# Optimization experiments

Hardware: AMD Instinct MI355X
Metric: run time of the kernel (lower is better)

The kernel has to match this reference:

```python
import jax, jax.numpy as jnp
import numpy as np

B, N, DIM = 4, 2048, 128
K = 32            # num_nearest_neighbors
FF = 4            # fourier_features
M_DIM = 16
EDGE_IN = FF * 2 + DIM * 2 + 1  # 265


def setup_inputs() -> dict:
    key = jax.random.key(0)
    ks = jax.random.split(key, 16)
    std = 0.001  # init_eps normal init for Linear weights
    p = {
        "feats": jax.random.normal(ks[0], (B, N, DIM), jnp.float32),
        "coors": jax.random.normal(ks[1], (B, N, 3), jnp.float32),
        # edge_mlp: Linear(265, 530) -> SiLU -> Linear(530, 16) -> SiLU
        "eW1": jax.random.normal(ks[2], (EDGE_IN, EDGE_IN * 2), jnp.float32) * std,
        "eb1": jax.random.normal(ks[3], (EDGE_IN * 2,), jnp.float32) * std,
        "eW2": jax.random.normal(ks[4], (EDGE_IN * 2, M_DIM), jnp.float32) * std,
        "eb2": jax.random.normal(ks[5], (M_DIM,), jnp.float32) * std,
        # coors_mlp: Linear(16, 64) -> SiLU -> Linear(64, 1)
        "cW1": jax.random.normal(ks[6], (M_DIM, M_DIM * 4), jnp.float32) * std,
        "cb1": jax.random.normal(ks[7], (M_DIM * 4,), jnp.float32) * std,
        "cW2": jax.random.normal(ks[8], (M_DIM * 4, 1), jnp.float32) * std,
        "cb2": jax.random.normal(ks[9], (1,), jnp.float32) * std,
        # node_mlp: Linear(144, 256) -> SiLU -> Linear(256, 128)
        "nW1": jax.random.normal(ks[10], (DIM + M_DIM, DIM * 2), jnp.float32) * std,
        "nb1": jax.random.normal(ks[11], (DIM * 2,), jnp.float32) * std,
        "nW2": jax.random.normal(ks[12], (DIM * 2, DIM), jnp.float32) * std,
        "nb2": jax.random.normal(ks[13], (DIM,), jnp.float32) * std,
    }
    return p


def _egnn_fwd(feats, coors, eW1, eb1, eW2, eb2, cW1, cb1, cW2, cb2, nW1, nb1, nW2, nb2):
    # all-pairs squared distances: [b, n, n]
    rel_coors_full = coors[:, :, None, :] - coors[:, None, :, :]
    rel_dist = jnp.sum(rel_coors_full * rel_coors_full, axis=-1)

    # top-k nearest (smallest distance) -> indices [b, n, k]
    _, idx = jax.lax.top_k(-rel_dist, K)

    # gather neighbor coords / feats per batch: [b, n, k, *]
    coors_j = jax.vmap(lambda x, i: x[i])(coors, idx)
    feats_j = jax.vmap(lambda x, i: x[i])(feats, idx)
    rel_coors = coors[:, :, None, :] - coors_j                     # b n k 3
    d = jnp.take_along_axis(rel_dist, idx, axis=2)[..., None]       # b n k 1

    # fourier encode distances: [b, n, k, 2*FF + 1]
    scales = 2.0 ** jnp.arange(FF, dtype=feats.dtype)               # [FF]
    xs = d[..., None] / scales                                      # b n k 1 FF
    enc = jnp.concatenate([jnp.sin(xs), jnp.cos(xs), d[..., None]], axis=-1)
    enc = enc[..., 0, :]                                            # b n k (2FF+1)

    feats_i = jnp.broadcast_to(feats[:, :, None, :], feats_j.shape)
    edge_input = jnp.concatenate([feats_i, feats_j, enc], axis=-1)  # b n k 265

    # edge MLP -> messages m_ij [b, n, k, m_dim]
    h = jax.nn.silu(edge_input @ eW1 + eb1)
    m_ij = jax.nn.silu(h @ eW2 + eb2)

    # coors MLP -> per-edge coordinate weights [b, n, k]
    cw = (jax.nn.silu(m_ij @ cW1 + cb1) @ cW2 + cb2)[..., 0]
    coors_out = jnp.einsum('bij,bijc->bic', cw, rel_coors) + coors

    # node update: sum-pool messages, concat with feats, MLP + residual
    m_i = jnp.sum(m_ij, axis=-2)                                    # b n m_dim
    node_in = jnp.concatenate([feats, m_i], axis=-1)
    node_out = jax.nn.silu(node_in @ nW1 + nb1) @ nW2 + nb2 + feats
    return node_out, coors_out


def reference(feats, coors, eW1, eb1, eW2, eb2, cW1, cb1, cW2, cb2, nW1, nb1, nW2, nb2):
    return _egnn_fwd(feats, coors, eW1, eb1, eW2, eb2, cW1, cb1, cW2, cb2, nW1, nb1, nW2, nb2)
```

## Files before the change

### kernel.cpp

```cpp
#include <hip/hip_runtime.h>
#include <hip/hip_bf16.h>
#include <math.h>

#define Bb 4
#define Nn 2048
#define DIMd 128
#define Kk 32
#define H1 530
#define PW2 530
#define MD 16
#define NDH 256
#define NDI 144
#define HSP 552

typedef float f32x2 __attribute__((ext_vector_type(2)));
typedef float f32x4 __attribute__((ext_vector_type(4)));
typedef short s16x8 __attribute__((ext_vector_type(8)));

__device__ __forceinline__ unsigned short f2bf(float f){
    union { float f; unsigned u; } v; v.f = f;
    unsigned r = v.u + 0x7FFFu + ((v.u >> 16) & 1u);
    return (unsigned short)(r >> 16);
}
__device__ __forceinline__ float silu_f(float x){
    float e = __builtin_amdgcn_exp2f(x * -1.442695041f);
    return x * __builtin_amdgcn_rcpf(1.0f + e);
}
__device__ __forceinline__ f32x2 silu2(f32x2 x){
    float e0 = __builtin_amdgcn_exp2f(x[0] * -1.442695041f);
    float e1 = __builtin_amdgcn_exp2f(x[1] * -1.442695041f);
    f32x2 r;
    r[0] = x[0] * __builtin_amdgcn_rcpf(1.0f + e0);
    r[1] = x[1] * __builtin_amdgcn_rcpf(1.0f + e1);
    return r;
}
__device__ __forceinline__ unsigned cvt_pk_bf16(float a, float b){
    unsigned r;
    asm("v_cvt_pk_bf16_f32 %0, %1, %2" : "=v"(r) : "v"(a), "v"(b));
    return r;
}

__global__ __launch_bounds__(256) void topk_kernel(const float* __restrict__ coors,
        int* __restrict__ idx_ws, float* __restrict__ dv_ws){
    int tid = threadIdx.x;
    int w = tid >> 6, lane = tid & 63;
    int node = blockIdx.x * 4 + w;
    int b = node >> 11;
    const float* cbp = coors + (size_t)b * Nn * 3;
    float cx = coors[node*3+0], cy = coors[node*3+1], cz = coors[node*3+2];
    float d[32];
    #pragma unroll
    for (int t = 0; t < 32; t++){
        int j = t*64 + lane;
        float dx = cx - cbp[j*3+0], dy = cy - cbp[j*3+1], dz = cz - cbp[j*3+2];
        d[t] = dx*dx + dy*dy + dz*dz;
    }
    float md = d[0]; int mj = lane;
    #pragma unroll
    for (int t = 1; t < 32; t++){
        int jt = t*64 + lane;
        if (d[t] < md){ md = d[t]; mj = jt; }
    }
    for (int r = 0; r < Kk; r++){
        float bd = md; int bj = mj;
        #pragma unroll
        for (int off = 32; off; off >>= 1){
            float d2 = __shfl_xor(bd, off); int j2 = __shfl_xor(bj, off);
            if (d2 < bd || (d2 == bd && j2 < bj)){ bd = d2; bj = j2; }
        }
        if (lane == 0){
            idx_ws[node*Kk + r] = bj;
            dv_ws[node*Kk + r] = bd;
        }
        if (mj == bj){
            md = 3.4e38f; mj = 0x7fffffff;
            #pragma unroll
            for (int t = 0; t < 32; t++){
                int jt = t*64 + lane;
                if (jt == bj) d[t] = 3.4e38f;
                if (d[t] < md){ md = d[t]; mj = jt; }
            }
        }
    }
}

__global__ __launch_bounds__(256) void fragw_kernel(const float* __restrict__ eW1,
        const float* __restrict__ eW2,
        unsigned short* __restrict__ W1F, unsigned short* __restrict__ WPF,
        unsigned short* __restrict__ W2F){
    int i0 = blockIdx.x * 256 + threadIdx.x;
    int stride = gridDim.x * 256;
    for (int i = i0; i < 34*5*512; i += stride){
        int j = i & 7, lane = (i >> 3) & 63, t = i >> 9;
        int ks = t % 5, nt = t / 5;
        int cg = nt*16 + (lane & 15);
        int k = ks*32 + ((lane >> 4) << 3) + j;
        float v = 0.f;
        if (cg < H1){
            if (k < 128) v = eW1[(size_t)(128+k)*H1 + cg];
            else if (k < 137) v = eW1[(size_t)(256+(k-128))*H1 + cg];
        }
        W1F[i] = f2bf(v);
    }
    for (int i = i0; i < 34*4*512; i += stride){
        int j = i & 7, lane = (i >> 3) & 63, t = i >> 9;
        int ks = t & 3, nt = t >> 2;
        int cg = nt*16 + (lane & 15);
        int k = ks*32 + ((lane >> 4) << 3) + j;
        float v = (cg < H1) ? eW1[(size_t)k*H1 + cg] : 0.f;
        WPF[i] = f2bf(v);
    }
    for (int i = i0; i < 17*512; i += stride){
        int j = i & 7, lane = (i >> 3) & 63, s = i >> 9;
        int k = s*32 + ((lane >> 4) << 3) + j;
        int col = lane & 15;
        W2F[i] = (k < H1) ? f2bf(eW2[(size_t)k*MD + col]) : (unsigned short)0;
    }
}

__global__ __launch_bounds__(256) void pmat_kernel(const float* __restrict__ feats,
        const unsigned short* __restrict__ WPF, const float* __restrict__ eb1,
        float* __restrict__ P){
    int tid = threadIdx.x;
    int wid = tid >> 6, lane = tid & 63;
    int node0 = blockIdx.x * 32;
    int kg = (lane >> 4) * 8;
    s16x8 af[2][4];
    #pragma unroll
    for (int m = 0; m < 2; m++){
        const float* fr = feats + (size_t)(node0 + m*16 + (lane & 15)) * DIMd;
        #pragma unroll
        for (int ks = 0; ks < 4; ks++){
            f32x4 lo = *(const f32x4*)(fr + ks*32 + kg);
            f32x4 hi = *(const f32x4*)(fr + ks*32 + kg + 4);
            union { s16x8 v; unsigned u[4]; } pk;
            pk.u[0] = cvt_pk_bf16(lo[0], lo[1]); pk.u[1] = cvt_pk_bf16(lo[2], lo[3]);
            pk.u[2] = cvt_pk_bf16(hi[0], hi[1]); pk.u[3] = cvt_pk_bf16(hi[2], hi[3]);
            af[m][ks] = pk.v;
        }
    }
    const s16x8* WPFv = (const s16x8*)WPF;
    for (int nt = wid; nt < 34; nt += 4){
        f32x4 acc0 = {0,0,0,0}, acc1 = {0,0,0,0};
        #pragma unroll
        for (int ks = 0; ks < 4; ks++){
            s16x8 bb = WPFv[(nt*4 + ks)*64 + lane];
            acc0 = __builtin_amdgcn_mfma_f32_16x16x32_bf16(af[0][ks], bb, acc0, 0, 0, 0);
            acc1 = __builtin_amdgcn_mfma_f32_16x16x32_bf16(af[1][ks], bb, acc1, 0, 0, 0);
        }
        int cg = nt*16 + (lane & 15);
        if (cg < H1){
            float b = eb1[cg];
            int r0 = (lane >> 4) * 4;
            #pragma unroll
            for (int r = 0; r < 4; r++){
                P[(size_t)(node0 + r0 + r)*PW2 + cg]      = acc0[r] + b;
                P[(size_t)(node0 + 16 + r0 + r)*PW2 + cg] = acc1[r] + b;
            }
        }
    }
}

__global__ __launch_bounds__(256, 4) void edge_kernel(const float* __restrict__ coors,
        const float* __restrict__ feats, const float* __restrict__ eb2,
        const float* __restrict__ cW1, const float* __restrict__ cb1,
        const float* __restrict__ cW2, const float* __restrict__ cb2,
        const float* __restrict__ P, const unsigned short* __restrict__ W1F,
        const unsigned short* __restrict__ W2F,
        const int* __restrict__ idx_ws, const float* __restrict__ dv_ws,
        float* __restrict__ mi_ws, float* __restrict__ coors_out){
    __shared__ unsigned short Hs[Kk][HSP];
    __shared__ float Pi_lds[544];
    __shared__ __align__(16) unsigned short aenc[Kk][32];
    __shared__ int js[Kk];
    __shared__ float rels[Kk][3];
    __shared__ float cacc[4][3];
    float (*m_s)[MD] = (float (*)[MD])aenc;

    int node = blockIdx.x; int tid = threadIdx.x;
    int b = node >> 11;
    int wid = tid >> 6, lane = tid & 63;

    const float* Pn = P + (size_t)node*PW2;
    Pi_lds[tid]       = Pn[tid];
    Pi_lds[tid + 256] = (tid + 256 < PW2) ? Pn[tid + 256] : 0.f;
    if (tid < 32) Pi_lds[512 + tid] = (512 + tid < PW2) ? Pn[512 + tid] : 0.f;
    if (tid < Kk){
        int j = idx_ws[node*Kk + tid];
        float dv = dv_ws[node*Kk + tid];
        js[tid] = j;
        unsigned short e[9];
        e[0] = f2bf(sinf(dv));        e[1] = f2bf(sinf(dv*0.5f));
        e[2] = f2bf(sinf(dv*0.25f));  e[3] = f2bf(sinf(dv*0.125f));
        e[4] = f2bf(cosf(dv));        e[5] = f2bf(cosf(dv*0.5f));
        e[6] = f2bf(cosf(dv*0.25f));  e[7] = f2bf(cosf(dv*0.125f));
        e[8] = f2bf(dv);
        #pragma unroll
        for (int q = 0; q < 9; q++) aenc[tid][q] = e[q];
        #pragma unroll
        for (int q = 9; q < 32; q++) aenc[tid][q] = 0;
        int jg = (b << 11) + j;
        rels[tid][0] = coors[node*3+0] - coors[jg*3+0];
        rels[tid][1] = coors[node*3+1] - coors[jg*3+1];
        rels[tid][2] = coors[node*3+2] - coors[jg*3+2];
    }
    __syncthreads();

    int kg = (lane >> 4) * 8;
    s16x8 af[2][5];
    #pragma unroll
    for (int m = 0; m < 2; m++){
        int row = m*16 + (lane & 15);
        int jgl = (b << 11) + js[row];
        const float* fr = feats + (size_t)jgl * DIMd;
        #pragma unroll
        for (int ks = 0; ks < 4; ks++){
            f32x4 lo = *(const f32x4*)(fr + ks*32 + kg);
            f32x4 hi = *(const f32x4*)(fr + ks*32 + kg + 4);
            union { s16x8 v; unsigned u[4]; } pk;
            pk.u[0] = cvt_pk_bf16(lo[0], lo[1]); pk.u[1] = cvt_pk_bf16(lo[2], lo[3]);
            pk.u[2] = cvt_pk_bf16(hi[0], hi[1]); pk.u[3] = cvt_pk_bf16(hi[2], hi[3]);
            af[m][ks] = pk.v;
        }
        af[m][4] = *(const s16x8*)(&aenc[row][kg]);
    }

    const s16x8* W1Fv = (const s16x8*)W1F;
    for (int nt = wid; nt < 34; nt += 4){
        f32x4 acc0 = {0,0,0,0}, acc1 = {0,0,0,0};
        #pragma unroll
        for (int ks = 0; ks < 5; ks++){
            s16x8 bb = W1Fv[(nt*5 + ks)*64 + lane];
            acc0 = __builtin_amdgcn_mfma_f32_16x16x32_bf16(af[0][ks], bb, acc0, 0, 0, 0);
            acc1 = __builtin_amdgcn_mfma_f32_16x16x32_bf16(af[1][ks], bb, acc1, 0, 0, 0);
        }
        int cg = nt*16 + (lane & 15);
        bool valid = cg < H1;
        float pic = Pi_lds[cg];
        int r0 = (lane >> 4) * 4;
        #pragma unroll
        for (int r = 0; r < 4; r++){
            float x0 = acc0[r] + pic, x1 = acc1[r] + pic;
            Hs[r0 + r][cg]      = valid ? f2bf(silu_f(x0)) : (unsigned short)0;
            Hs[16 + r0 + r][cg] = valid ? f2bf(silu_f(x1)) : (unsigned short)0;
        }
    }
    __syncthreads();

    if (wid < 2){
        f32x4 acc = {0.f,0.f,0.f,0.f};
        int ar = wid*16 + (lane & 15);
        const s16x8* W2Fv = (const s16x8*)W2F;
        for (int s = 0; s < 17; s++){
            s16x8 a  = *(const s16x8*)(&Hs[ar][s*32 + kg]);
            s16x8 bb = W2Fv[s*64 + lane];
            acc = __builtin_amdgcn_mfma_f32_16x16x32_bf16(a, bb, acc, 0, 0, 0);
        }
        int col = lane & 15, r0 = (lane >> 4) * 4;
        #pragma unroll
        for (int r = 0; r < 4; r++) m_s[wid*16 + r0 + r][col] = acc[r];
    }
    __syncthreads();
    for (int t = tid; t < Kk*MD; t += 256){
        int n = t >> 4, f = t & 15;
        m_s[n][f] = silu_f(m_s[n][f] + eb2[f]);
    }
    __syncthreads();
    if (tid < MD){
        float s = 0.f;
        for (int n = 0; n < Kk; n++) s += m_s[n][tid];
        mi_ws[node*MD + tid] = s;
    }
    float ax = 0.f, ay = 0.f, az = 0.f;
    for (int q = 0; q < 8; q++){
        int n = wid*8 + q;
        float acc = cb1[lane];
        #pragma unroll
        for (int f = 0; f < MD; f++) acc += m_s[n][f] * cW1[f*64 + lane];
        float p = silu_f(acc) * cW2[lane];
        #pragma unroll
        for (int off = 32; off; off >>= 1) p += __shfl_xor(p, off);
        float cw = p + cb2[0];
        ax += cw * rels[n][0];
        ay += cw * rels[n][1];
        az += cw * rels[n][2];
    }
    if (lane == 0){ cacc[wid][0] = ax; cacc[wid][1] = ay; cacc[wid][2] = az; }
    __syncthreads();
    if (tid == 0){
        coors_out[node*3+0] = cacc[0][0]+cacc[1][0]+cacc[2][0]+cacc[3][0] + coors[node*3+0];
        coors_out[node*3+1] = cacc[0][1]+cacc[1][1]+cacc[2][1]+cacc[3][1] + coors[node*3+1];
        coors_out[node*3+2] = cacc[0][2]+cacc[1][2]+cacc[2][2]+cacc[3][2] + coors[node*3+2];
    }
}

__global__ __launch_bounds__(256) void node_kernel(const float* __restrict__ feats,
        const float* __restrict__ mi_ws,
        const float* __restrict__ nW1, const float* __restrict__ nb1,
        const float* __restrict__ nW2, const float* __restrict__ nb2,
        float* __restrict__ out){
    __shared__ float insT[NDI][12];
    __shared__ float hsdT[NDH][12];
    int tid = threadIdx.x;
    int node0 = blockIdx.x * 8;
    for (int t = tid; t < 8*DIMd; t += 256){
        int m = t >> 7, k = t & 127;
        insT[k][m] = feats[(size_t)node0*DIMd + t];
    }
    if (tid < 8*MD) insT[DIMd + (tid & 15)][tid >> 4] = mi_ws[node0*MD + tid];
    __syncthreads();
    float bias = nb1[tid];
    f32x2 acc[4];
    #pragma unroll
    for (int p = 0; p < 4; p++) acc[p] = (f32x2){bias, bias};
    for (int k = 0; k < NDI; k++){
        float wv = nW1[(size_t)k*NDH + tid];
        f32x2 w2 = {wv, wv};
        acc[0] += *(const f32x2*)&insT[k][0] * w2;
        acc[1] += *(const f32x2*)&insT[k][2] * w2;
        acc[2] += *(const f32x2*)&insT[k][4] * w2;
        acc[3] += *(const f32x2*)&insT[k][6] * w2;
    }
    #pragma unroll
    for (int p = 0; p < 4; p++) *(f32x2*)&hsdT[tid][2*p] = silu2(acc[p]);
    __syncthreads();
    int c = tid & 127, half = tid >> 7;
    float b2 = nb2[c];
    f32x2 a0 = {b2, b2}, a1 = {b2, b2};
    for (int k = 0; k < NDH; k++){
        float wv = nW2[(size_t)k*DIMd + c];
        f32x2 w2 = {wv, wv};
        a0 += *(const f32x2*)&hsdT[k][half*4]     * w2;
        a1 += *(const f32x2*)&hsdT[k][half*4 + 2] * w2;
    }
    #pragma unroll
    for (int q = 0; q < 4; q++){
        int m = half*4 + q;
        float v = (q < 2) ? a0[q & 1] : a1[q & 1];
        out[(size_t)(node0+m)*DIMd + c] = v + feats[(size_t)(node0+m)*DIMd + c];
    }
}

extern "C" void kernel_launch(void* const* d_in, const int* in_sizes, int n_in,
                              void* d_out, int out_size, void* d_ws, size_t ws_size,
                              hipStream_t stream){
    const float* feats = (const float*)d_in[0];
    const float* coors = (const float*)d_in[1];
    const float* eW1 = (const float*)d_in[2];
    const float* eb1 = (const float*)d_in[3];
    const float* eW2 = (const float*)d_in[4];
    const float* eb2 = (const float*)d_in[5];
    const float* cW1 = (const float*)d_in[6];
    const float* cb1 = (const float*)d_in[7];
    const float* cW2 = (const float*)d_in[8];
    const float* cb2 = (const float*)d_in[9];
    const float* nW1 = (const float*)d_in[10];
    const float* nb1 = (const float*)d_in[11];
    const float* nW2 = (const float*)d_in[12];
    const float* nb2 = (const float*)d_in[13];
    float* out = (float*)d_out;
    float* coors_out = out + (size_t)Bb*Nn*DIMd;

    char* ws = (char*)d_ws;
    int*   idx_ws = (int*)ws;
    float* dv_ws  = (float*)(ws + (1u<<20));
    float* Pd     = (float*)(ws + (2u<<20));
    float* mi_ws  = (float*)(ws + (2u<<20) + 17367040u);
    unsigned short* W1F = (unsigned short*)(ws + (2u<<20) + 17367040u + 524288u);
    unsigned short* WPF = (unsigned short*)(ws + (2u<<20) + 17367040u + 524288u + 174080u);
    unsigned short* W2F = (unsigned short*)(ws + (2u<<20) + 17367040u + 524288u + 174080u + 139264u);

    fragw_kernel<<<256, 256, 0, stream>>>(eW1, eW2, W1F, WPF, W2F);
    pmat_kernel<<<Bb*Nn/32, 256, 0, stream>>>(feats, WPF, eb1, Pd);
    topk_kernel<<<Bb*Nn/4, 256, 0, stream>>>(coors, idx_ws, dv_ws);
    edge_kernel<<<Bb*Nn, 256, 0, stream>>>(coors, feats, eb2, cW1, cb1, cW2, cb2,
                                           Pd, W1F, W2F, idx_ws, dv_ws, mi_ws, coors_out);
    node_kernel<<<Bb*Nn/8, 256, 0, stream>>>(feats, mi_ws, nW1, nb1, nW2, nb2, out);
}
```

Baseline: 305.0 us.

## Split edge kernel into two half-neighbor blocks per node with partial-sum combine

Each node's 32 neighbors are now handled by two blocks of 16 edges. Each block writes partial message sums and partial coordinate updates, and a new combine kernel plus the node kernel add the two halves together. The change halves per-block LDS and registers, raises the occupancy hint to 8, stores the P bias row as bf16, and vectorises the coors-MLP across 16-lane groups. The cost is that every W1 fragment load now feeds only one MFMA instead of two, which doubles W1 global traffic, and an extra kernel launch is added. Rounding the bias to bf16 also adds precision loss.

```diff
diff --git a/kernel.cpp b/kernel.cpp
--- a/kernel.cpp
+++ b/kernel.cpp
@@ -21,6 +21,10 @@
     union { float f; unsigned u; } v; v.f = f;
     unsigned r = v.u + 0x7FFFu + ((v.u >> 16) & 1u);
     return (unsigned short)(r >> 16);
+}
+__device__ __forceinline__ float bf2f(unsigned short u){
+    union { unsigned u; float f; } v; v.u = ((unsigned)u) << 16;
+    return v.f;
 }
 __device__ __forceinline__ float silu_f(float x){
     float e = __builtin_amdgcn_exp2f(x * -1.442695041f);
@@ -161,33 +165,35 @@
     }
 }
 
-__global__ __launch_bounds__(256, 4) void edge_kernel(const float* __restrict__ coors,
+__global__ __launch_bounds__(256, 8) void edge_kernel(const float* __restrict__ coors,
         const float* __restrict__ feats, const float* __restrict__ eb2,
         const float* __restrict__ cW1, const float* __restrict__ cb1,
         const float* __restrict__ cW2, const float* __restrict__ cb2,
         const float* __restrict__ P, const unsigned short* __restrict__ W1F,
         const unsigned short* __restrict__ W2F,
         const int* __restrict__ idx_ws, const float* __restrict__ dv_ws,
-        float* __restrict__ mi_ws, float* __restrict__ coors_out){
-    __shared__ unsigned short Hs[Kk][HSP];
-    __shared__ float Pi_lds[544];
-    __shared__ __align__(16) unsigned short aenc[Kk][32];
-    __shared__ int js[Kk];
-    __shared__ float rels[Kk][3];
+        float* __restrict__ mi_part, float* __restrict__ co_part){
+    __shared__ unsigned short Hs[16][HSP];
+    __shared__ unsigned short Pi_bf[544];
+    __shared__ __align__(16) unsigned short aenc[16][32];
+    __shared__ int js[16];
+    __shared__ float rels[16][3];
     __shared__ float cacc[4][3];
     float (*m_s)[MD] = (float (*)[MD])aenc;
 
-    int node = blockIdx.x; int tid = threadIdx.x;
+    int bid = blockIdx.x;
+    int node = bid >> 1, h = bid & 1;
     int b = node >> 11;
+    int tid = threadIdx.x;
     int wid = tid >> 6, lane = tid & 63;
 
     const float* Pn = P + (size_t)node*PW2;
-    Pi_lds[tid]       = Pn[tid];
-    Pi_lds[tid + 256] = (tid + 256 < PW2) ? Pn[tid + 256] : 0.f;
-    if (tid < 32) Pi_lds[512 + tid] = (512 + tid < PW2) ? Pn[512 + tid] : 0.f;
-    if (tid < Kk){
-        int j = idx_ws[node*Kk + tid];
-        float dv = dv_ws[node*Kk + tid];
+    Pi_bf[tid] = f2bf(Pn[tid]);
+    { int c = tid + 256; Pi_bf[c] = (c < PW2) ? f2bf(Pn[c]) : (unsigned short)0; }
+    if (tid < 32){ int c = 512 + tid; Pi_bf[c] = (c < PW2) ? f2bf(Pn[c]) : (unsigned short)0; }
+    if (tid < 16){
+        int j = idx_ws[node*Kk + h*16 + tid];
+        float dv = dv_ws[node*Kk + h*16 + tid];
         js[tid] = j;
         unsigned short e[9];
         e[0] = f2bf(sinf(dv));        e[1] = f2bf(sinf(dv*0.5f));
@@ -207,10 +213,9 @@
     __syncthreads();
 
     int kg = (lane >> 4) * 8;
-    s16x8 af[2][5];
-    #pragma unroll
-    for (int m = 0; m < 2; m++){
-        int row = m*16 + (lane & 15);
+    int row = lane & 15;
+    s16x8 af[5];
+    {
         int jgl = (b << 11) + js[row];
         const float* fr = feats + (size_t)jgl * DIMd;
         #pragma unroll
@@ -220,36 +225,32 @@
             union { s16x8 v; unsigned u[4]; } pk;
             pk.u[0] = cvt_pk_bf16(lo[0], lo[1]); pk.u[1] = cvt_pk_bf16(lo[2], lo[3]);
             pk.u[2] = cvt_pk_bf16(hi[0], hi[1]); pk.u[3] = cvt_pk_bf16(hi[2], hi[3]);
-            af[m][ks] = pk.v;
-        }
-        af[m][4] = *(const s16x8*)(&aenc[row][kg]);
+            af[ks] = pk.v;
+        }
+        af[4] = *(const s16x8*)(&aenc[row][kg]);
     }
 
     const s16x8* W1Fv = (const s16x8*)W1F;
     for (int nt = wid; nt < 34; nt += 4){
-        f32x4 acc0 = {0,0,0,0}, acc1 = {0,0,0,0};
+        f32x4 acc = {0,0,0,0};
         #pragma unroll
         for (int ks = 0; ks < 5; ks++){
             s16x8 bb = W1Fv[(nt*5 + ks)*64 + lane];
-            acc0 = __builtin_amdgcn_mfma_f32_16x16x32_bf16(af[0][ks], bb, acc0, 0, 0, 0);
-            acc1 = __builtin_amdgcn_mfma_f32_16x16x32_bf16(af[1][ks], bb, acc1, 0, 0, 0);
+            acc = __builtin_amdgcn_mfma_f32_16x16x32_bf16(af[ks], bb, acc, 0, 0, 0);
         }
         int cg = nt*16 + (lane & 15);
         bool valid = cg < H1;
-        float pic = Pi_lds[cg];
+        float pic = bf2f(Pi_bf[cg]);
         int r0 = (lane >> 4) * 4;
         #pragma unroll
-        for (int r = 0; r < 4; r++){
-            float x0 = acc0[r] + pic, x1 = acc1[r] + pic;
-            Hs[r0 + r][cg]      = valid ? f2bf(silu_f(x0)) : (unsigned short)0;
-            Hs[16 + r0 + r][cg] = valid ? f2bf(silu_f(x1)) : (unsigned short)0;
-        }
-    }
-    __syncthreads();
-
-    if (wid < 2){
+        for (int r = 0; r < 4; r++)
+            Hs[r0 + r][cg] = valid ? f2bf(silu_f(acc[r] + pic)) : (unsigned short)0;
+    }
+    __syncthreads();
+
+    if (wid == 0){
         f32x4 acc = {0.f,0.f,0.f,0.f};
-        int ar = wid*16 + (lane & 15);
+        int ar = lane & 15;
         const s16x8* W2Fv = (const s16x8*)W2F;
         for (int s = 0; s < 17; s++){
             s16x8 a  = *(const s16x8*)(&Hs[ar][s*32 + kg]);
@@ -258,44 +259,58 @@
         }
         int col = lane & 15, r0 = (lane >> 4) * 4;
         #pragma unroll
-        for (int r = 0; r < 4; r++) m_s[wid*16 + r0 + r][col] = acc[r];
-    }
-    __syncthreads();
-    for (int t = tid; t < Kk*MD; t += 256){
-        int n = t >> 4, f = t & 15;
-        m_s[n][f] = silu_f(m_s[n][f] + eb2[f]);
-    }
+        for (int r = 0; r < 4; r++) m_s[r0 + r][col] = acc[r];
+    }
+    __syncthreads();
+    { int n = tid >> 4, f = tid & 15; m_s[n][f] = silu_f(m_s[n][f] + eb2[f]); }
     __syncthreads();
     if (tid < MD){
         float s = 0.f;
-        for (int n = 0; n < Kk; n++) s += m_s[n][tid];
-        mi_ws[node*MD + tid] = s;
-    }
-    float ax = 0.f, ay = 0.f, az = 0.f;
-    for (int q = 0; q < 8; q++){
-        int n = wid*8 + q;
-        float acc = cb1[lane];
-        #pragma unroll
-        for (int f = 0; f < MD; f++) acc += m_s[n][f] * cW1[f*64 + lane];
-        float p = silu_f(acc) * cW2[lane];
-        #pragma unroll
-        for (int off = 32; off; off >>= 1) p += __shfl_xor(p, off);
-        float cw = p + cb2[0];
-        ax += cw * rels[n][0];
-        ay += cw * rels[n][1];
-        az += cw * rels[n][2];
-    }
-    if (lane == 0){ cacc[wid][0] = ax; cacc[wid][1] = ay; cacc[wid][2] = az; }
+        #pragma unroll
+        for (int n = 0; n < 16; n++) s += m_s[n][tid];
+        mi_part[bid*MD + tid] = s;
+    }
+    int eid = wid*4 + (lane >> 4);
+    int u4 = (lane & 15) * 4;
+    f32x4 acc4 = *(const f32x4*)(cb1 + u4);
+    #pragma unroll
+    for (int f = 0; f < MD; f++){
+        float mv = m_s[eid][f];
+        f32x4 w4 = *(const f32x4*)(cW1 + f*64 + u4);
+        acc4 += (f32x4){mv,mv,mv,mv} * w4;
+    }
+    f32x4 c24 = *(const f32x4*)(cW2 + u4);
+    float p = silu_f(acc4[0])*c24[0] + silu_f(acc4[1])*c24[1]
+            + silu_f(acc4[2])*c24[2] + silu_f(acc4[3])*c24[3];
+    #pragma unroll
+    for (int off = 1; off < 16; off <<= 1) p += __shfl_xor(p, off);
+    float cw = p + cb2[0];
+    bool owner = (lane & 15) == 0;
+    float vx = owner ? cw * rels[eid][0] : 0.f;
+    float vy = owner ? cw * rels[eid][1] : 0.f;
+    float vz = owner ? cw * rels[eid][2] : 0.f;
+    vx += __shfl_xor(vx, 16); vx += __shfl_xor(vx, 32);
+    vy += __shfl_xor(vy, 16); vy += __shfl_xor(vy, 32);
+    vz += __shfl_xor(vz, 16); vz += __shfl_xor(vz, 32);
+    if (lane == 0){ cacc[wid][0] = vx; cacc[wid][1] = vy; cacc[wid][2] = vz; }
     __syncthreads();
     if (tid == 0){
-        coors_out[node*3+0] = cacc[0][0]+cacc[1][0]+cacc[2][0]+cacc[3][0] + coors[node*3+0];
-        coors_out[node*3+1] = cacc[0][1]+cacc[1][1]+cacc[2][1]+cacc[3][1] + coors[node*3+1];
-        coors_out[node*3+2] = cacc[0][2]+cacc[1][2]+cacc[2][2]+cacc[3][2] + coors[node*3+2];
-    }
+        co_part[bid*3+0] = cacc[0][0]+cacc[1][0]+cacc[2][0]+cacc[3][0];
+        co_part[bid*3+1] = cacc[0][1]+cacc[1][1]+cacc[2][1]+cacc[3][1];
+        co_part[bid*3+2] = cacc[0][2]+cacc[1][2]+cacc[2][2]+cacc[3][2];
+    }
+}
+
+__global__ __launch_bounds__(256) void combine_kernel(const float* __restrict__ coors,
+        const float* __restrict__ co_part, float* __restrict__ coors_out){
+    int i = blockIdx.x * 256 + threadIdx.x;
+    if (i >= Bb*Nn*3) return;
+    int n = i / 3, c = i - n*3;
+    coors_out[i] = co_part[(n*2)*3 + c] + co_part[(n*2+1)*3 + c] + coors[i];
 }
 
 __global__ __launch_bounds__(256) void node_kernel(const float* __restrict__ feats,
-        const float* __restrict__ mi_ws,
+        const float* __restrict__ mi_part,
         const float* __restrict__ nW1, const float* __restrict__ nb1,
         const float* __restrict__ nW2, const float* __restrict__ nb2,
         float* __restrict__ out){
@@ -307,7 +322,11 @@
         int m = t >> 7, k = t & 127;
         insT[k][m] = feats[(size_t)node0*DIMd + t];
     }
-    if (tid < 8*MD) insT[DIMd + (tid & 15)][tid >> 4] = mi_ws[node0*MD + tid];
+    if (tid < 8*MD){
+        int m = tid >> 4, f = tid & 15;
+        insT[DIMd + f][m] = mi_part[(size_t)(node0+m)*32 + f]
+                          + mi_part[(size_t)(node0+m)*32 + 16 + f];
+    }
     __syncthreads();
     float bias = nb1[tid];
     f32x2 acc[4];
@@ -362,18 +381,21 @@
     float* coors_out = out + (size_t)Bb*Nn*DIMd;
 
     char* ws = (char*)d_ws;
-    int*   idx_ws = (int*)ws;
-    float* dv_ws  = (float*)(ws + (1u<<20));
-    float* Pd     = (float*)(ws + (2u<<20));
-    float* mi_ws  = (float*)(ws + (2u<<20) + 17367040u);
-    unsigned short* W1F = (unsigned short*)(ws + (2u<<20) + 17367040u + 524288u);
-    unsigned short* WPF = (unsigned short*)(ws + (2u<<20) + 17367040u + 524288u + 174080u);
-    unsigned short* W2F = (unsigned short*)(ws + (2u<<20) + 17367040u + 524288u + 174080u + 139264u);
+    size_t off = 0;
+    int*   idx_ws = (int*)(ws + off);   off += (1u<<20);
+    float* dv_ws  = (float*)(ws + off); off += (1u<<20);
+    float* Pd     = (float*)(ws + off); off += 17367040u;
+    float* mi_part= (float*)(ws + off); off += (1u<<20);
+    float* co_part= (float*)(ws + off); off += 196608u;
+    unsigned short* W1F = (unsigned short*)(ws + off); off += 174080u;
+    unsigned short* WPF = (unsigned short*)(ws + off); off += 139264u;
+    unsigned short* W2F = (unsigned short*)(ws + off); off += 17408u;
 
     fragw_kernel<<<256, 256, 0, stream>>>(eW1, eW2, W1F, WPF, W2F);
     pmat_kernel<<<Bb*Nn/32, 256, 0, stream>>>(feats, WPF, eb1, Pd);
     topk_kernel<<<Bb*Nn/4, 256, 0, stream>>>(coors, idx_ws, dv_ws);
-    edge_kernel<<<Bb*Nn, 256, 0, stream>>>(coors, feats, eb2, cW1, cb1, cW2, cb2,
-                                           Pd, W1F, W2F, idx_ws, dv_ws, mi_ws, coors_out);
-    node_kernel<<<Bb*Nn/8, 256, 0, stream>>>(feats, mi_ws, nW1, nb1, nW2, nb2, out);
-}
+    edge_kernel<<<Bb*Nn*2, 256, 0, stream>>>(coors, feats, eb2, cW1, cb1, cW2, cb2,
+                                             Pd, W1F, W2F, idx_ws, dv_ws, mi_part, co_part);
+    combine_kernel<<<(Bb*Nn*3 + 255)/256, 256, 0, stream>>>(coors, co_part, coors_out);
+    node_kernel<<<Bb*Nn/8, 256, 0, stream>>>(feats, mi_part, nW1, nb1, nW2, nb2, out);
+}
```

Result: slower. 345.8 us (+13.4%).

## Fuse second edge-MLP layer into first-layer tile loop, drop hidden LDS buffer

Applied to the files above, without the earlier changes.

The edge kernel no longer stores the full 32x530 bf16 hidden activation in shared memory. Each wave now writes its 16x16 SiLU tile to a small per-wave buffer and immediately multiplies it by a zero-padded W2 fragment, accumulating partial messages that are reduced across waves through LDS. The idle two-wave second GEMM and one barrier are removed, and the lower LDS use allows a launch-bounds occupancy hint of 5. The coors MLP is also reworked to use 4-wide vector math with 16-lane reductions. The trade-off is that half of each second-layer MFMA multiplies padding zeros, and every tile adds extra LDS round trips.

```diff
diff --git a/kernel.cpp b/kernel.cpp
--- a/kernel.cpp
+++ b/kernel.cpp
@@ -11,10 +11,10 @@
 #define MD 16
 #define NDH 256
 #define NDI 144
-#define HSP 552
 
 typedef float f32x2 __attribute__((ext_vector_type(2)));
 typedef float f32x4 __attribute__((ext_vector_type(4)));
+typedef short s16x4 __attribute__((ext_vector_type(4)));
 typedef short s16x8 __attribute__((ext_vector_type(8)));
 
 __device__ __forceinline__ unsigned short f2bf(float f){
@@ -87,7 +87,7 @@
 __global__ __launch_bounds__(256) void fragw_kernel(const float* __restrict__ eW1,
         const float* __restrict__ eW2,
         unsigned short* __restrict__ W1F, unsigned short* __restrict__ WPF,
-        unsigned short* __restrict__ W2F){
+        unsigned short* __restrict__ W2F2){
     int i0 = blockIdx.x * 256 + threadIdx.x;
     int stride = gridDim.x * 256;
     for (int i = i0; i < 34*5*512; i += stride){
@@ -110,11 +110,13 @@
         float v = (cg < H1) ? eW1[(size_t)k*H1 + cg] : 0.f;
         WPF[i] = f2bf(v);
     }
-    for (int i = i0; i < 17*512; i += stride){
-        int j = i & 7, lane = (i >> 3) & 63, s = i >> 9;
-        int k = s*32 + ((lane >> 4) << 3) + j;
+    for (int i = i0; i < 34*512; i += stride){
+        int j = i & 7, lane = (i >> 3) & 63, nt = i >> 9;
+        int kl = ((lane >> 4) << 3) + j;
         int col = lane & 15;
-        W2F[i] = (k < H1) ? f2bf(eW2[(size_t)k*MD + col]) : (unsigned short)0;
+        int row = nt*16 + kl;
+        float v = (kl < 16 && row < H1) ? eW2[(size_t)row*MD + col] : 0.f;
+        W2F2[i] = f2bf(v);
     }
 }
 
@@ -161,30 +163,35 @@
     }
 }
 
-__global__ __launch_bounds__(256, 4) void edge_kernel(const float* __restrict__ coors,
+#define TS 24
+__global__ __launch_bounds__(256, 5) void edge_kernel(const float* __restrict__ coors,
         const float* __restrict__ feats, const float* __restrict__ eb2,
         const float* __restrict__ cW1, const float* __restrict__ cb1,
         const float* __restrict__ cW2, const float* __restrict__ cb2,
         const float* __restrict__ P, const unsigned short* __restrict__ W1F,
-        const unsigned short* __restrict__ W2F,
+        const unsigned short* __restrict__ W2F2,
         const int* __restrict__ idx_ws, const float* __restrict__ dv_ws,
         float* __restrict__ mi_ws, float* __restrict__ coors_out){
-    __shared__ unsigned short Hs[Kk][HSP];
     __shared__ float Pi_lds[544];
     __shared__ __align__(16) unsigned short aenc[Kk][32];
     __shared__ int js[Kk];
     __shared__ float rels[Kk][3];
+    __shared__ unsigned short T[4][16][TS];
+    __shared__ float m_red[4][Kk][MD];
     __shared__ float cacc[4][3];
-    float (*m_s)[MD] = (float (*)[MD])aenc;
 
     int node = blockIdx.x; int tid = threadIdx.x;
     int b = node >> 11;
     int wid = tid >> 6, lane = tid & 63;
 
+    for (int t = tid; t < 4*16*(TS-16); t += 256){
+        int w = t / (16*(TS-16)), rem = t % (16*(TS-16));
+        T[w][rem / (TS-16)][16 + rem % (TS-16)] = 0;
+    }
     const float* Pn = P + (size_t)node*PW2;
     Pi_lds[tid]       = Pn[tid];
-    Pi_lds[tid + 256] = (tid + 256 < PW2) ? Pn[tid + 256] : 0.f;
-    if (tid < 32) Pi_lds[512 + tid] = (512 + tid < PW2) ? Pn[512 + tid] : 0.f;
+    { int c = tid + 256; Pi_lds[c] = (c < PW2) ? Pn[c] : 0.f; }
+    if (tid < 32){ int c = 512 + tid; Pi_lds[c] = (c < PW2) ? Pn[c] : 0.f; }
     if (tid < Kk){
         int j = idx_ws[node*Kk + tid];
         float dv = dv_ws[node*Kk + tid];
@@ -207,6 +214,7 @@
     __syncthreads();
 
     int kg = (lane >> 4) * 8;
+    int kga = (kg >= 16) ? 16 : kg;
     s16x8 af[2][5];
     #pragma unroll
     for (int m = 0; m < 2; m++){
@@ -225,7 +233,10 @@
         af[m][4] = *(const s16x8*)(&aenc[row][kg]);
     }
 
-    const s16x8* W1Fv = (const s16x8*)W1F;
+    const s16x8* W1Fv  = (const s16x8*)W1F;
+    const s16x8* W2F2v = (const s16x8*)W2F2;
+    f32x4 macc0 = {0,0,0,0}, macc1 = {0,0,0,0};
+    int col = lane & 15, r0 = (lane >> 4) * 4;
     for (int nt = wid; nt < 34; nt += 4){
         f32x4 acc0 = {0,0,0,0}, acc1 = {0,0,0,0};
         #pragma unroll
@@ -234,58 +245,77 @@
             acc0 = __builtin_amdgcn_mfma_f32_16x16x32_bf16(af[0][ks], bb, acc0, 0, 0, 0);
             acc1 = __builtin_amdgcn_mfma_f32_16x16x32_bf16(af[1][ks], bb, acc1, 0, 0, 0);
         }
-        int cg = nt*16 + (lane & 15);
+        int cg = nt*16 + col;
         bool valid = cg < H1;
         float pic = Pi_lds[cg];
-        int r0 = (lane >> 4) * 4;
-        #pragma unroll
-        for (int r = 0; r < 4; r++){
-            float x0 = acc0[r] + pic, x1 = acc1[r] + pic;
-            Hs[r0 + r][cg]      = valid ? f2bf(silu_f(x0)) : (unsigned short)0;
-            Hs[16 + r0 + r][cg] = valid ? f2bf(silu_f(x1)) : (unsigned short)0;
-        }
-    }
-    __syncthreads();
-
-    if (wid < 2){
-        f32x4 acc = {0.f,0.f,0.f,0.f};
-        int ar = wid*16 + (lane & 15);
-        const s16x8* W2Fv = (const s16x8*)W2F;
-        for (int s = 0; s < 17; s++){
-            s16x8 a  = *(const s16x8*)(&Hs[ar][s*32 + kg]);
-            s16x8 bb = W2Fv[s*64 + lane];
-            acc = __builtin_amdgcn_mfma_f32_16x16x32_bf16(a, bb, acc, 0, 0, 0);
-        }
-        int col = lane & 15, r0 = (lane >> 4) * 4;
-        #pragma unroll
-        for (int r = 0; r < 4; r++) m_s[wid*16 + r0 + r][col] = acc[r];
-    }
-    __syncthreads();
+        s16x8 w2b = W2F2v[nt*64 + lane];
+        #pragma unroll
+        for (int r = 0; r < 4; r++)
+            T[wid][r0 + r][col] = valid ? f2bf(silu_f(acc0[r] + pic)) : (unsigned short)0;
+        {
+            union { s16x8 v; s16x4 h[2]; } a2;
+            a2.h[0] = *(const s16x4*)&T[wid][col][kga];
+            a2.h[1] = *(const s16x4*)&T[wid][col][kga + 4];
+            macc0 = __builtin_amdgcn_mfma_f32_16x16x32_bf16(a2.v, w2b, macc0, 0, 0, 0);
+        }
+        #pragma unroll
+        for (int r = 0; r < 4; r++)
+            T[wid][r0 + r][col] = valid ? f2bf(silu_f(acc1[r] + pic)) : (unsigned short)0;
+        {
+            union { s16x8 v; s16x4 h[2]; } a2;
+            a2.h[0] = *(const s16x4*)&T[wid][col][kga];
+            a2.h[1] = *(const s16x4*)&T[wid][col][kga + 4];
+            macc1 = __builtin_amdgcn_mfma_f32_16x16x32_bf16(a2.v, w2b, macc1, 0, 0, 0);
+        }
+    }
+    #pragma unroll
+    for (int r = 0; r < 4; r++){
+        m_red[wid][r0 + r][col]      = macc0[r];
+        m_red[wid][16 + r0 + r][col] = macc1[r];
+    }
+    __syncthreads();
+    #pragma unroll
     for (int t = tid; t < Kk*MD; t += 256){
         int n = t >> 4, f = t & 15;
-        m_s[n][f] = silu_f(m_s[n][f] + eb2[f]);
+        float s = m_red[0][n][f] + m_red[1][n][f] + m_red[2][n][f] + m_red[3][n][f];
+        m_red[0][n][f] = silu_f(s + eb2[f]);
     }
     __syncthreads();
     if (tid < MD){
         float s = 0.f;
-        for (int n = 0; n < Kk; n++) s += m_s[n][tid];
+        #pragma unroll
+        for (int n = 0; n < Kk; n++) s += m_red[0][n][tid];
         mi_ws[node*MD + tid] = s;
     }
-    float ax = 0.f, ay = 0.f, az = 0.f;
-    for (int q = 0; q < 8; q++){
-        int n = wid*8 + q;
-        float acc = cb1[lane];
-        #pragma unroll
-        for (int f = 0; f < MD; f++) acc += m_s[n][f] * cW1[f*64 + lane];
-        float p = silu_f(acc) * cW2[lane];
-        #pragma unroll
-        for (int off = 32; off; off >>= 1) p += __shfl_xor(p, off);
+    float vx = 0.f, vy = 0.f, vz = 0.f;
+    int u4 = col * 4;
+    f32x4 cb14 = *(const f32x4*)(cb1 + u4);
+    f32x4 c24  = *(const f32x4*)(cW2 + u4);
+    #pragma unroll
+    for (int q = 0; q < 2; q++){
+        int eid = wid*8 + (lane >> 4)*2 + q;
+        f32x4 acc4 = cb14;
+        #pragma unroll
+        for (int f = 0; f < MD; f++){
+            float mv = m_red[0][eid][f];
+            f32x4 w4 = *(const f32x4*)(cW1 + f*64 + u4);
+            acc4 += (f32x4){mv,mv,mv,mv} * w4;
+        }
+        float p = silu_f(acc4[0])*c24[0] + silu_f(acc4[1])*c24[1]
+                + silu_f(acc4[2])*c24[2] + silu_f(acc4[3])*c24[3];
+        #pragma unroll
+        for (int off = 1; off < 16; off <<= 1) p += __shfl_xor(p, off);
         float cw = p + cb2[0];
-        ax += cw * rels[n][0];
-        ay += cw * rels[n][1];
-        az += cw * rels[n][2];
-    }
-    if (lane == 0){ cacc[wid][0] = ax; cacc[wid][1] = ay; cacc[wid][2] = az; }
+        if (col == 0){
+            vx += cw * rels[eid][0];
+            vy += cw * rels[eid][1];
+            vz += cw * rels[eid][2];
+        }
+    }
+    vx += __shfl_xor(vx, 16); vx += __shfl_xor(vx, 32);
+    vy += __shfl_xor(vy, 16); vy += __shfl_xor(vy, 32);
+    vz += __shfl_xor(vz, 16); vz += __shfl_xor(vz, 32);
+    if (lane == 0){ cacc[wid][0] = vx; cacc[wid][1] = vy; cacc[wid][2] = vz; }
     __syncthreads();
     if (tid == 0){
         coors_out[node*3+0] = cacc[0][0]+cacc[1][0]+cacc[2][0]+cacc[3][0] + coors[node*3+0];
@@ -362,18 +392,19 @@
     float* coors_out = out + (size_t)Bb*Nn*DIMd;
 
     char* ws = (char*)d_ws;
-    int*   idx_ws = (int*)ws;
-    float* dv_ws  = (float*)(ws + (1u<<20));
-    float* Pd     = (float*)(ws + (2u<<20));
-    float* mi_ws  = (float*)(ws + (2u<<20) + 17367040u);
-    unsigned short* W1F = (unsigned short*)(ws + (2u<<20) + 17367040u + 524288u);
-    unsigned short* WPF = (unsigned short*)(ws + (2u<<20) + 17367040u + 524288u + 174080u);
-    unsigned short* W2F = (unsigned short*)(ws + (2u<<20) + 17367040u + 524288u + 174080u + 139264u);
-
-    fragw_kernel<<<256, 256, 0, stream>>>(eW1, eW2, W1F, WPF, W2F);
+    size_t off = 0;
+    int*   idx_ws = (int*)(ws + off);   off += (1u<<20);
+    float* dv_ws  = (float*)(ws + off); off += (1u<<20);
+    float* Pd     = (float*)(ws + off); off += 17367040u;
+    float* mi_ws  = (float*)(ws + off); off += 524288u;
+    unsigned short* W1F  = (unsigned short*)(ws + off); off += 174080u;
+    unsigned short* WPF  = (unsigned short*)(ws + off); off += 139264u;
+    unsigned short* W2F2 = (unsigned short*)(ws + off); off += 34816u;
+
+    fragw_kernel<<<256, 256, 0, stream>>>(eW1, eW2, W1F, WPF, W2F2);
     pmat_kernel<<<Bb*Nn/32, 256, 0, stream>>>(feats, WPF, eb1, Pd);
     topk_kernel<<<Bb*Nn/4, 256, 0, stream>>>(coors, idx_ws, dv_ws);
     edge_kernel<<<Bb*Nn, 256, 0, stream>>>(coors, feats, eb2, cW1, cb1, cW2, cb2,
-                                           Pd, W1F, W2F, idx_ws, dv_ws, mi_ws, coors_out);
+                                           Pd, W1F, W2F2, idx_ws, dv_ws, mi_ws, coors_out);
     node_kernel<<<Bb*Nn/8, 256, 0, stream>>>(feats, mi_ws, nW1, nb1, nW2, nb2, out);
 }
```

After: 304.9 us. No clear change (-0.0%).
